# Kernel optimization log

Measured on AMD Instinct MI355X. Metric: run time of the kernel, lower is better.

The kernel has to match this reference:

```python
import jax, jax.numpy as jnp
import numpy as np

B, S, H = 4, 2048, 2048
E, K = 4, 2
FF = 4 * H  # standard MLP expert expansion


def setup_inputs() -> dict:
    key = jax.random.key(0)
    ks = jax.random.split(key, 5)
    sc = 0.02
    return {
        "hidden_states": jax.random.normal(ks[0], (B, S, H), jnp.float32),
        "w_gate": jax.random.normal(ks[1], (H, E), jnp.float32) * sc,
        "b_gate": jnp.zeros((E,), jnp.float32),
        "w1": jax.random.normal(ks[2], (E, H, FF), jnp.float32) * sc,
        "b1": jnp.zeros((E, FF), jnp.float32),
        "w2": jax.random.normal(ks[3], (E, FF, H), jnp.float32) * sc,
        "b2": jnp.zeros((E, H), jnp.float32),
    }


def reference(hidden_states, w_gate, b_gate, w1, b1, w2, b2):
    # Router: linear gate -> softmax -> top-k, renormalized gate weights
    logits = jnp.einsum("bsh,he->bse", hidden_states, w_gate) + b_gate
    probs = jax.nn.softmax(logits, axis=-1)                       # [B,S,E]
    top_p, top_i = jax.lax.top_k(probs, K)                        # [B,S,K]
    gate_w = top_p / jnp.sum(top_p, axis=-1, keepdims=True)

    # Switch-style load-balancing aux loss
    route = jax.nn.one_hot(top_i, E, dtype=probs.dtype)           # [B,S,K,E]
    frac_tokens = jnp.mean(jnp.sum(route, axis=2) / K, axis=(0, 1))  # [E]
    mean_prob = jnp.mean(probs, axis=(0, 1))                      # [E]
    aux_loss = E * jnp.sum(frac_tokens * mean_prob)

    # Dispatch/combine: small fixed expert count -> loop over experts,
    # dense FFN on all tokens, mask via gate weight (0 for unrouted tokens).
    out = jnp.zeros_like(hidden_states)
    for e in range(E):
        w_e = jnp.sum(gate_w * (top_i == e), axis=-1)             # [B,S]
        h = jax.nn.gelu(jnp.einsum("bsh,hf->bsf", hidden_states, w1[e]) + b1[e])
        y = jnp.einsum("bsf,fh->bsh", h, w2[e]) + b2[e]
        out = out + w_e[..., None] * y
    return out, aux_loss
```

## Files before the change

### kernel.cpp

```cpp
#include <hip/hip_runtime.h>

typedef unsigned short u16;
typedef __attribute__((ext_vector_type(8))) short bf16x8;
typedef __attribute__((ext_vector_type(4))) float f32x4;

#define TOK  8192
#define HD   2048
#define FFD  8192
#define NEXP 4
#define CAPE 4352

__device__ __forceinline__ u16 f2bf(float f){
  unsigned u = __float_as_uint(f);
  u += 0x7fffu + ((u >> 16) & 1u);
  return (u16)(u >> 16);
}

__device__ __forceinline__ float gelu_tanh(float x){
  float u = 0.7978845608028654f * (x + 0.044715f * x * x * x);
  return 0.5f * x * (1.0f + tanhf(u));
}

__device__ __forceinline__ void gload_lds16(const void* g, void* l){
  __builtin_amdgcn_global_load_lds((const __attribute__((address_space(1))) void*)g,
                                   (__attribute__((address_space(3))) void*)l, 16, 0, 0);
}

__device__ __forceinline__ f32x4 mfma_bf16(bf16x8 a, bf16x8 b, f32x4 c){
  asm("v_mfma_f32_16x16x32_bf16 %0, %1, %2, %0" : "+v"(c) : "v"(a), "v"(b));
  return c;
}

__global__ __launch_bounds__(256) void cvt_to_bf16(const float* __restrict__ in,
                                                   u16* __restrict__ out, int n4){
  int i = blockIdx.x * 256 + threadIdx.x;
  if (i >= n4) return;
  float4 v = ((const float4*)in)[i];
  ushort4 o;
  o.x = f2bf(v.x); o.y = f2bf(v.y); o.z = f2bf(v.z); o.w = f2bf(v.w);
  ((ushort4*)out)[i] = o;
}

__global__ __launch_bounds__(256) void transpose_cvt(const float* __restrict__ in,
                                                     u16* __restrict__ out, int R, int C){
  __shared__ float tile[64][65];
  int tx = threadIdx.x & 63;
  int ty = threadIdx.x >> 6;
  size_t r0 = (size_t)blockIdx.y * 64;
  size_t c0 = (size_t)blockIdx.x * 64;
  #pragma unroll
  for (int i = ty; i < 64; i += 4)
    tile[i][tx] = in[(r0 + i) * C + (c0 + tx)];
  __syncthreads();
  #pragma unroll
  for (int i = ty; i < 64; i += 4)
    out[(c0 + i) * R + (r0 + tx)] = f2bf(tile[tx][i]);
}

__global__ __launch_bounds__(256) void router_kernel(
    const float* __restrict__ X, const float* __restrict__ wg, const float* __restrict__ bg,
    float* __restrict__ probs, int* __restrict__ topi, float* __restrict__ gatew){
  int t = blockIdx.x;
  const float* x = X + (size_t)t * HD;
  float a0 = 0.f, a1 = 0.f, a2 = 0.f, a3 = 0.f;
  for (int h = threadIdx.x; h < HD; h += 256){
    float xv = x[h];
    float4 w = ((const float4*)wg)[h];
    a0 += xv * w.x; a1 += xv * w.y; a2 += xv * w.z; a3 += xv * w.w;
  }
  __shared__ float red[4][256];
  red[0][threadIdx.x] = a0; red[1][threadIdx.x] = a1;
  red[2][threadIdx.x] = a2; red[3][threadIdx.x] = a3;
  __syncthreads();
  for (int s = 128; s > 0; s >>= 1){
    if (threadIdx.x < (unsigned)s){
      #pragma unroll
      for (int e = 0; e < 4; e++) red[e][threadIdx.x] += red[e][threadIdx.x + s];
    }
    __syncthreads();
  }
  if (threadIdx.x == 0){
    float l[4], p[4];
    #pragma unroll
    for (int e = 0; e < 4; e++) l[e] = red[e][0] + bg[e];
    float mx = fmaxf(fmaxf(l[0], l[1]), fmaxf(l[2], l[3]));
    float s = 0.f;
    #pragma unroll
    for (int e = 0; e < 4; e++){ p[e] = expf(l[e] - mx); s += p[e]; }
    #pragma unroll
    for (int e = 0; e < 4; e++){ p[e] /= s; probs[t * 4 + e] = p[e]; }
    int e0 = 0;
    for (int e = 1; e < 4; e++) if (p[e] > p[e0]) e0 = e;
    int e1 = -1;
    for (int e = 0; e < 4; e++){ if (e == e0) continue; if (e1 < 0 || p[e] > p[e1]) e1 = e; }
    float g = p[e0] + p[e1];
    topi[t * 2] = e0; topi[t * 2 + 1] = e1;
    #pragma unroll
    for (int e = 0; e < 4; e++)
      gatew[(size_t)e * TOK + t] = (e == e0) ? p[e0] / g : (e == e1) ? p[e1] / g : 0.f;
  }
}

__global__ __launch_bounds__(256) void build_lists(const int* __restrict__ topi,
                                                   int* __restrict__ cnt,
                                                   int* __restrict__ lists){
  int t = blockIdx.x * 256 + threadIdx.x;
  if (t >= TOK) return;
  #pragma unroll
  for (int k = 0; k < 2; k++){
    int e = topi[t * 2 + k];
    int p = atomicAdd(cnt + e, 1);
    lists[e * TOK + p] = t;
  }
}

__global__ __launch_bounds__(256) void aux_kernel(const float* __restrict__ probs,
                                                  const int* __restrict__ topi,
                                                  float* __restrict__ out_aux){
  __shared__ float sp[4][256];
  __shared__ float sc[4][256];
  float p[4] = {0,0,0,0}, c[4] = {0,0,0,0};
  for (int t = threadIdx.x; t < TOK; t += 256){
    #pragma unroll
    for (int e = 0; e < 4; e++) p[e] += probs[t * 4 + e];
    c[topi[t * 2]]     += 1.f;
    c[topi[t * 2 + 1]] += 1.f;
  }
  #pragma unroll
  for (int e = 0; e < 4; e++){ sp[e][threadIdx.x] = p[e]; sc[e][threadIdx.x] = c[e]; }
  __syncthreads();
  for (int s = 128; s > 0; s >>= 1){
    if (threadIdx.x < (unsigned)s){
      #pragma unroll
      for (int e = 0; e < 4; e++){
        sp[e][threadIdx.x] += sp[e][threadIdx.x + s];
        sc[e][threadIdx.x] += sc[e][threadIdx.x + s];
      }
    }
    __syncthreads();
  }
  if (threadIdx.x == 0){
    float aux = 0.f;
    #pragma unroll
    for (int e = 0; e < 4; e++)
      aux += (sc[e][0] / (float)(TOK * 2)) * (sp[e][0] / (float)TOK);
    *out_aux = 4.f * aux;
  }
}

template<int EPI, int N, int K>
__global__ __launch_bounds__(256) void gemm_97(
    const u16* __restrict__ A, const u16* __restrict__ BT,
    const int* __restrict__ rowidx, const int* __restrict__ cntp,
    const float* __restrict__ bias,
    u16* __restrict__ Hout,
    const float* __restrict__ gate, float* __restrict__ Cout)
{
  __shared__ __align__(16) u16 As[128 * 64];
  __shared__ __align__(16) u16 Bs[128 * 64];
  const int Mv = *cntp;
  const int nwg = gridDim.x * gridDim.y;
  const int orig = blockIdx.x + gridDim.x * blockIdx.y;
  const int q8 = nwg >> 3, r8 = nwg & 7, xcd = orig & 7, rank = orig >> 3;
  const int v = (xcd < r8 ? xcd * (q8 + 1) : r8 * (q8 + 1) + (xcd - r8) * q8) + rank;
  const int bx = v % (int)gridDim.x, by = v / (int)gridDim.x;
  const int browg = by * 128;
  if (browg >= Mv) return;
  const size_t bcol = (size_t)bx * 128;

  const int tid = threadIdx.x, lane = tid & 63, w = tid >> 6;
  const int wr = w >> 1, wc = w & 1;
  const int l8 = lane >> 3;
  const int csw  = ((lane & 7) ^ l8) * 8;
  const int sw   = (lane & 7) * 8;
  const int h8   = ((lane >> 4) & 3) * 8;
  const int colk0 = h8 ^ sw, colk1 = (32 | h8) ^ sw;
  const int r16 = lane & 15;

  const u16* bsrc[4]; int bch[4];
  #pragma unroll
  for (int j = 0; j < 4; j++){
    int rb = j * 32 + w * 8;
    bch[j] = rb * 128;
    bsrc[j] = BT + (bcol + rb + l8) * (size_t)K + csw;
  }
  const u16* asrc[4]; int ach[4];
  #pragma unroll
  for (int q = 0; q < 4; q++){
    int rb = wr * 64 + q * 16 + wc * 8;
    ach[q] = rb * 128;
    int rl = browg + rb + l8;
    int ar;
    if (EPI == 0){
      if (rl > Mv - 1) rl = Mv - 1;
      ar = rowidx[rl];
    } else {
      ar = rl;
    }
    asrc[q] = A + (size_t)ar * K + csw;
  }

  f32x4 acc[4][4];
  #pragma unroll
  for (int m = 0; m < 4; m++)
    #pragma unroll
    for (int n = 0; n < 4; n++) acc[m][n] = (f32x4){0.f, 0.f, 0.f, 0.f};
  bf16x8 bC[8];

  const int NT = K / 64;
  for (int t = 0; t < NT; ++t){
    const size_t ko = (size_t)t * 64;
    __syncthreads();
    #pragma unroll
    for (int j = 0; j < 4; j++) gload_lds16(bsrc[j] + ko, (char*)Bs + bch[j]);
    #pragma unroll
    for (int q = 0; q < 4; q++) gload_lds16(asrc[q] + ko, (char*)As + ach[q]);
    __syncthreads();

    #pragma unroll
    for (int nf = 0; nf < 4; nf++){
      const u16* bp = Bs + (wc * 64 + nf * 16 + r16) * 64;
      bC[nf * 2]     = *(const bf16x8*)(bp + colk0);
      bC[nf * 2 + 1] = *(const bf16x8*)(bp + colk1);
    }
    #pragma unroll
    for (int m = 0; m < 4; m++){
      const u16* ap = As + (wr * 64 + m * 16 + r16) * 64;
      bf16x8 a0 = *(const bf16x8*)(ap + colk0);
      bf16x8 a1 = *(const bf16x8*)(ap + colk1);
      #pragma unroll
      for (int nf = 0; nf < 4; nf++){
        acc[m][nf] = mfma_bf16(a0, bC[nf * 2],     acc[m][nf]);
        acc[m][nf] = mfma_bf16(a1, bC[nf * 2 + 1], acc[m][nf]);
      }
    }
  }

  const int cl = r16, rg = (lane >> 4) * 4;
  const size_t c0 = bcol + wc * 64;
  float bv[4];
  #pragma unroll
  for (int nf = 0; nf < 4; nf++) bv[nf] = bias[c0 + nf * 16 + cl];
  #pragma unroll
  for (int mf = 0; mf < 4; mf++){
    const int rbase = browg + wr * 64 + mf * 16 + rg;
    if (EPI == 0){
      #pragma unroll
      for (int nf = 0; nf < 4; nf++){
        const size_t col = c0 + nf * 16 + cl;
        #pragma unroll
        for (int j = 0; j < 4; j++)
          Hout[(size_t)(rbase + j) * N + col] = f2bf(gelu_tanh(acc[mf][nf][j] + bv[nf]));
      }
    } else {
      int   tok[4]; float gv[4];
      #pragma unroll
      for (int j = 0; j < 4; j++){
        const bool ok = (rbase + j) < Mv;
        tok[j] = ok ? rowidx[rbase + j] : -1;
        gv[j]  = ok ? gate[tok[j]] : 0.f;
      }
      #pragma unroll
      for (int nf = 0; nf < 4; nf++){
        const size_t col = c0 + nf * 16 + cl;
        #pragma unroll
        for (int j = 0; j < 4; j++){
          if (tok[j] >= 0){
            const size_t idx = (size_t)tok[j] * N + col;
            Cout[idx] += gv[j] * (acc[mf][nf][j] + bv[nf]);
          }
        }
      }
    }
  }
}

extern "C" void kernel_launch(void* const* d_in, const int* in_sizes, int n_in,
                              void* d_out, int out_size, void* d_ws, size_t ws_size,
                              hipStream_t stream){
  (void)in_sizes; (void)n_in; (void)ws_size;
  const float* X  = (const float*)d_in[0];
  const float* wg = (const float*)d_in[1];
  const float* bg = (const float*)d_in[2];
  const float* w1 = (const float*)d_in[3];
  const float* b1 = (const float*)d_in[4];
  const float* w2 = (const float*)d_in[5];
  const float* b2 = (const float*)d_in[6];
  float* out = (float*)d_out;

  char* ws = (char*)d_ws;
  size_t off = 0;
  auto alloc = [&](size_t b) -> char* {
    char* p = ws + off;
    off = (off + b + 255) & ~(size_t)255;
    return p;
  };
  u16*   Xb    = (u16*)  alloc((size_t)TOK * HD * 2);
  u16*   W1T   = (u16*)  alloc((size_t)FFD * HD * 2);
  u16*   W2T   = (u16*)  alloc((size_t)HD * FFD * 2);
  float* probs = (float*)alloc((size_t)TOK * 4 * 4);
  int*   topi  = (int*)  alloc((size_t)TOK * 2 * 4);
  float* gatew = (float*)alloc((size_t)NEXP * TOK * 4);
  int*   cnt   = (int*)  alloc((size_t)NEXP * 4);
  int*   lists = (int*)  alloc((size_t)NEXP * TOK * 4);
  u16*   Hb    = (u16*)  alloc((size_t)CAPE * FFD * 2);

  hipMemsetAsync(cnt, 0, NEXP * sizeof(int), stream);
  hipMemsetAsync(out, 0, (size_t)TOK * HD * sizeof(float), stream);

  cvt_to_bf16<<<(TOK * HD / 4 + 255) / 256, 256, 0, stream>>>(X, Xb, TOK * HD / 4);
  router_kernel<<<TOK, 256, 0, stream>>>(X, wg, bg, probs, topi, gatew);
  build_lists<<<TOK / 256, 256, 0, stream>>>(topi, cnt, lists);
  aux_kernel<<<1, 256, 0, stream>>>(probs, topi, out + (out_size - 1));

  for (int e = 0; e < NEXP; ++e){
    transpose_cvt<<<dim3(FFD / 64, HD / 64), 256, 0, stream>>>(
        w1 + (size_t)e * HD * FFD, W1T, HD, FFD);
    transpose_cvt<<<dim3(HD / 64, FFD / 64), 256, 0, stream>>>(
        w2 + (size_t)e * FFD * HD, W2T, FFD, HD);
    gemm_97<0, FFD, HD><<<dim3(FFD / 128, CAPE / 128), 256, 0, stream>>>(
        Xb, W1T, lists + e * TOK, cnt + e, b1 + (size_t)e * FFD,
        Hb, nullptr, nullptr);
    gemm_97<1, HD, FFD><<<dim3(HD / 128, CAPE / 128), 256, 0, stream>>>(
        Hb, W2T, lists + e * TOK, cnt + e, b2 + (size_t)e * HD,
        nullptr, gatew + (size_t)e * TOK, out);
  }
}
```

Before: 1.830 ms.

## Widen transpose tiles with bf16 LDS staging and remap GEMM blocks per XCD

```diff
diff --git a/kernel.cpp b/kernel.cpp
--- a/kernel.cpp
+++ b/kernel.cpp
@@ -43,18 +43,25 @@
 
 __global__ __launch_bounds__(256) void transpose_cvt(const float* __restrict__ in,
                                                      u16* __restrict__ out, int R, int C){
-  __shared__ float tile[64][65];
-  int tx = threadIdx.x & 63;
-  int ty = threadIdx.x >> 6;
-  size_t r0 = (size_t)blockIdx.y * 64;
-  size_t c0 = (size_t)blockIdx.x * 64;
-  #pragma unroll
-  for (int i = ty; i < 64; i += 4)
-    tile[i][tx] = in[(r0 + i) * C + (c0 + tx)];
+  __shared__ u16 t[64][138];
+  const int tx = threadIdx.x & 63;
+  const int w  = threadIdx.x >> 6;
+  const size_t r0 = (size_t)blockIdx.y * 128;
+  const size_t c0 = (size_t)blockIdx.x * 64;
+  #pragma unroll
+  for (int i = 0; i < 32; i++){
+    const int r = w * 32 + i;
+    t[tx][r] = f2bf(in[(r0 + r) * C + c0 + tx]);
+  }
   __syncthreads();
   #pragma unroll
-  for (int i = ty; i < 64; i += 4)
-    out[(c0 + i) * R + (r0 + tx)] = f2bf(tile[tx][i]);
+  for (int j = 0; j < 16; j++){
+    const int c = j * 4 + w;
+    ushort2 o;
+    o.x = t[c][2 * tx];
+    o.y = t[c][2 * tx + 1];
+    *(ushort2*)(out + (c0 + c) * (size_t)R + r0 + 2 * tx) = o;
+  }
 }
 
 __global__ __launch_bounds__(256) void router_kernel(
@@ -159,11 +166,11 @@
   __shared__ __align__(16) u16 As[128 * 64];
   __shared__ __align__(16) u16 Bs[128 * 64];
   const int Mv = *cntp;
-  const int nwg = gridDim.x * gridDim.y;
-  const int orig = blockIdx.x + gridDim.x * blockIdx.y;
-  const int q8 = nwg >> 3, r8 = nwg & 7, xcd = orig & 7, rank = orig >> 3;
-  const int v = (xcd < r8 ? xcd * (q8 + 1) : r8 * (q8 + 1) + (xcd - r8) * q8) + rank;
-  const int bx = v % (int)gridDim.x, by = v / (int)gridDim.x;
+  const int gx = gridDim.x, gy = gridDim.y;
+  const int orig = blockIdx.x + gx * blockIdx.y;
+  const int xcd = orig & 7, rank = orig >> 3;
+  const int bxl = rank / gy, by = rank % gy;
+  const int bx = xcd * (gx >> 3) + bxl;
   const int browg = by * 128;
   if (browg >= Mv) return;
   const size_t bcol = (size_t)bx * 128;
@@ -314,9 +321,9 @@
   aux_kernel<<<1, 256, 0, stream>>>(probs, topi, out + (out_size - 1));
 
   for (int e = 0; e < NEXP; ++e){
-    transpose_cvt<<<dim3(FFD / 64, HD / 64), 256, 0, stream>>>(
+    transpose_cvt<<<dim3(FFD / 64, HD / 128), 256, 0, stream>>>(
         w1 + (size_t)e * HD * FFD, W1T, HD, FFD);
-    transpose_cvt<<<dim3(HD / 64, FFD / 64), 256, 0, stream>>>(
+    transpose_cvt<<<dim3(HD / 64, FFD / 128), 256, 0, stream>>>(
         w2 + (size_t)e * FFD * HD, W2T, FFD, HD);
     gemm_97<0, FFD, HD><<<dim3(FFD / 128, CAPE / 128), 256, 0, stream>>>(
         Xb, W1T, lists + e * TOK, cnt + e, b1 + (size_t)e * FFD,
```

Result: faster. 1.694 ms (-7.4%).
